# Kernel optimization log

Measured on AMD Instinct MI355X. Metric: run time of the kernel, lower is better.

Reference implementation:

```python
import jax, jax.numpy as jnp
import numpy as np

DIN = 1024   # input_embedding_size
D = 128      # embedding_size
N, T = 4, 4096


def setup_inputs() -> dict:
    key = jax.random.key(0)
    kx, kq, kk, kv = jax.random.split(key, 4)
    x = jax.random.normal(kx, (N, T, DIN), dtype=jnp.float32)
    # torch Linear(DIN, D, bias=False): weight [D, DIN], y = x @ W.T.
    # Store transposed [DIN, D] so q = x @ Wq is the same math.
    s = 1.0 / np.sqrt(DIN)
    Wq = jax.random.uniform(kq, (DIN, D), jnp.float32, -s, s)
    Wk = jax.random.uniform(kk, (DIN, D), jnp.float32, -s, s)
    Wv = jax.random.uniform(kv, (DIN, D), jnp.float32, -s, s)
    return {"x": x, "Wq": Wq, "Wk": Wk, "Wv": Wv}


def reference(x, Wq, Wk, Wv):
    # x: [N,T,DIN]
    q = jnp.einsum('ntc,cd->ntd', x, Wq)  # [N,T,D]
    k = jnp.einsum('ntc,cd->ntd', x, Wk)
    v = jnp.einsum('ntc,cd->ntd', x, Wv)
    att = jnp.einsum('ntd,nsd->nts', q, k)  # [N,T,T], no 1/sqrt(D) scaling (faithful)
    Tlen = x.shape[1]
    causal = jnp.tril(jnp.ones((Tlen, Tlen), dtype=bool))
    # faithful to torch: tril() zeros upper triangle, then masked_fill(att == 0, -inf)
    att = jnp.where(causal, att, 0.0)
    att = jnp.where(att == 0.0, -jnp.inf, att)
    att = jax.nn.softmax(att, axis=-1)  # [N,T,T]
    out = jnp.einsum('nts,nsd->ntd', att, v)  # [N,T,D]
    return out, att
```

## Files before the change

### kernel.cpp

```cpp
#include <hip/hip_runtime.h>

typedef _Float16 f16;
typedef __attribute__((ext_vector_type(8))) _Float16 f16x8;
typedef __attribute__((ext_vector_type(8))) short s16x8;
typedef __attribute__((ext_vector_type(4))) float f32x4;
typedef __attribute__((ext_vector_type(4))) unsigned short us16x4;

#define DIN   1024
#define DD    128
#define NBAT  4
#define TLEN  4096

static __device__ __forceinline__ unsigned short f2bf(float f) {
  unsigned int u = __builtin_bit_cast(unsigned int, f);
  u = (u + 0x7fffu + ((u >> 16) & 1u)) >> 16;
  return (unsigned short)u;
}
static __device__ __forceinline__ float bf2f(unsigned short h) {
  return __builtin_bit_cast(float, (unsigned int)h << 16);
}
static __device__ __forceinline__ unsigned short f2h(float f) {
  _Float16 h = (_Float16)f;
  return __builtin_bit_cast(unsigned short, h);
}
static __device__ __forceinline__ int swz128(int d, int key) {
  return ((((d >> 3) ^ key) & 15) << 3) | (d & 7);
}

typedef __attribute__((address_space(1))) const unsigned int* gas1_t;
typedef __attribute__((address_space(3))) unsigned int* las3_t;
static __device__ __forceinline__ void gload16(const void* g, void* l) {
  __builtin_amdgcn_global_load_lds((gas1_t)g, (las3_t)l, 16, 0, 0);
}

__global__ void build_wt(const float* __restrict__ Wq, const float* __restrict__ Wk,
                         const float* __restrict__ Wv,
                         unsigned short* __restrict__ Wh, unsigned short* __restrict__ Wl) {
  int col = blockIdx.x;
  const float* W = (col < 128) ? Wq : (col < 256 ? Wk : Wv);
  int j = col & 127;
  for (int kk = (int)threadIdx.x; kk < DIN; kk += blockDim.x) {
    float w = W[(size_t)kk * DD + j];
    unsigned short h = f2bf(w);
    unsigned short l = f2bf(w - bf2f(h));
    Wh[(size_t)col * DIN + kk] = h;
    Wl[(size_t)col * DIN + kk] = l;
  }
}

__global__ __launch_bounds__(256, 2) void proj_qkv(
    const float* __restrict__ x,
    const unsigned short* __restrict__ Wh, const unsigned short* __restrict__ Wl,
    unsigned short* __restrict__ qws, unsigned short* __restrict__ kws,
    unsigned short* __restrict__ vws) {
  __shared__ __align__(16) unsigned short Ah[32 * 64];
  __shared__ __align__(16) unsigned short Al[32 * 64];
  __shared__ __align__(16) unsigned short vt[128 * 40];

  const int tid = (int)threadIdx.x;
  const int lane = tid & 63;
  const int wid = tid >> 6;
  const int lr = lane & 15;
  const int lg = lane >> 4;
  const int t0 = blockIdx.x * 32;

  const int srow = tid >> 3;
  const int sg = tid & 7;
  const float* xsrc = x + (size_t)(t0 + srow) * DIN + sg * 8;
  const int sgs = (sg ^ (srow & 7)) * 8;

  f32x4 acc[2][6];
#pragma unroll
  for (int a = 0; a < 2; ++a)
#pragma unroll
    for (int c = 0; c < 6; ++c) acc[a][c] = f32x4{0.f, 0.f, 0.f, 0.f};

  for (int kr = 0; kr < 16; ++kr) {
    {
      f32x4 a0 = *(const f32x4*)(xsrc + kr * 64);
      f32x4 a1 = *(const f32x4*)(xsrc + kr * 64 + 4);
      s16x8 hv, lv;
#pragma unroll
      for (int e = 0; e < 4; ++e) {
        unsigned short h0 = f2bf(a0[e]);
        hv[e] = (short)h0; lv[e] = (short)f2bf(a0[e] - bf2f(h0));
        unsigned short h1 = f2bf(a1[e]);
        hv[4 + e] = (short)h1; lv[4 + e] = (short)f2bf(a1[e] - bf2f(h1));
      }
      *(s16x8*)&Ah[srow * 64 + sgs] = hv;
      *(s16x8*)&Al[srow * 64 + sgs] = lv;
    }
    __syncthreads();

#pragma unroll
    for (int kc = 0; kc < 2; ++kc) {
      s16x8 ah[2], al[2];
#pragma unroll
      for (int rf = 0; rf < 2; ++rf) {
        int g = (((kc * 4 + lg) ^ (lr & 7)) << 3);
        ah[rf] = *(const s16x8*)&Ah[(rf * 16 + lr) * 64 + g];
        al[rf] = *(const s16x8*)&Al[(rf * 16 + lr) * 64 + g];
      }
#pragma unroll
      for (int cf = 0; cf < 6; ++cf) {
        size_t boff = (size_t)(wid * 96 + cf * 16 + lr) * DIN + (size_t)kr * 64 + kc * 32 + lg * 8;
        s16x8 bh = *(const s16x8*)(Wh + boff);
        s16x8 bl = *(const s16x8*)(Wl + boff);
#pragma unroll
        for (int rf = 0; rf < 2; ++rf) {
          acc[rf][cf] = __builtin_amdgcn_mfma_f32_16x16x32_bf16(ah[rf], bh, acc[rf][cf], 0, 0, 0);
          acc[rf][cf] = __builtin_amdgcn_mfma_f32_16x16x32_bf16(ah[rf], bl, acc[rf][cf], 0, 0, 0);
          acc[rf][cf] = __builtin_amdgcn_mfma_f32_16x16x32_bf16(al[rf], bh, acc[rf][cf], 0, 0, 0);
        }
      }
    }
    __syncthreads();
  }

  const int n = t0 >> 12, t0l = t0 & (TLEN - 1);
#pragma unroll
  for (int cf = 0; cf < 6; ++cf) {
    int c = wid * 96 + cf * 16 + lr;
#pragma unroll
    for (int rf = 0; rf < 2; ++rf)
#pragma unroll
      for (int e = 0; e < 4; ++e) {
        int tl = rf * 16 + lg * 4 + e;
        int t = t0 + tl;
        unsigned short hv = f2h(acc[rf][cf][e]);
        if (c < 128) {
          qws[(size_t)t * DD + c] = hv;
        } else if (c < 256) {
          kws[(size_t)t * DD + swz128(c - 128, t & 7)] = hv;
        } else {
          vt[(c - 256) * 40 + tl] = hv;
        }
      }
  }
  __syncthreads();
  if (tid < 128) {
    int d = tid;
    unsigned short* dst = vws + ((size_t)n * DD + d) * TLEN + t0l;
#pragma unroll
    for (int h = 0; h < 4; ++h) {
      f16x8 vv = *(const f16x8*)&vt[d * 40 + h * 8];
      *(f16x8*)(dst + h * 8) = vv;
    }
  }
}

__global__ __launch_bounds__(512, 4) void attn_fused(
    const unsigned short* __restrict__ qws, const unsigned short* __restrict__ kws,
    const unsigned short* __restrict__ vws, float* __restrict__ out,
    float* __restrict__ att) {
  __shared__ __align__(16) unsigned short kl[2][16384];
  __shared__ __align__(16) unsigned short pp[8][16 * 40];
  __shared__ float zb[8][16];
  __shared__ float rzb[32];

  const int tid = (int)threadIdx.x;
  const int lane = tid & 63;
  const int wid = tid >> 6;
  const int lr = lane & 15;
  const int lg = lane >> 4;
  const int rg = wid >> 2;
  const int cg = wid & 3;

  int b = (int)blockIdx.x;
  int cr = (b < 256) ? b : (767 - b);
  const int qi = cr >> 2;
  const int n = cr & 3;
  const int t0 = qi * 32;
  const int jmax = (t0 + 31) >> 7;

  const unsigned short* kbase = kws + (size_t)(n * TLEN) * DD;
  const unsigned short* vbase = vws + (size_t)n * DD * TLEN;
  float* attn_base = att + (size_t)n * TLEN * TLEN + (size_t)t0 * TLEN;

#pragma unroll
  for (int rr = 0; rr < 4; ++rr) {
    int idx = rr * 512 + tid;
    gload16((const char*)kbase + (size_t)idx * 16, (char*)kl[0] + (size_t)idx * 16);
  }

  {
    int cz0 = (jmax + 1) * 128;
    f32x4 zv = f32x4{0.f, 0.f, 0.f, 0.f};
    for (int r = 0; r < 32; ++r) {
      float* rowp = attn_base + (size_t)r * TLEN;
      for (int c = cz0 + tid * 4; c < TLEN; c += 2048) *(f32x4*)(rowp + c) = zv;
    }
  }

  f16x8 qa[4];
  {
    const unsigned short* q0 = qws + (size_t)(n * TLEN + t0 + rg * 16 + lr) * DD + lg * 8;
#pragma unroll
    for (int kc = 0; kc < 4; ++kc) qa[kc] = *(const f16x8*)(q0 + kc * 32);
  }
  const int rowl0 = rg * 16 + lg * 4;

  float zacc[4] = {0.f, 0.f, 0.f, 0.f};
  for (int j = 0; j <= jmax; ++j) {
    __syncthreads();
    if (j < jmax) {
      const char* gk = (const char*)(kbase + (size_t)((j + 1) * 128) * DD);
#pragma unroll
      for (int rr = 0; rr < 4; ++rr) {
        int idx = rr * 512 + tid;
        gload16(gk + (size_t)idx * 16, (char*)kl[(j + 1) & 1] + (size_t)idx * 16);
      }
    }
    const unsigned short* klc = kl[j & 1];
#pragma unroll
    for (int cf = 0; cf < 2; ++cf) {
      int krow = cg * 32 + cf * 16 + lr;
      f32x4 s = f32x4{0.f, 0.f, 0.f, 0.f};
#pragma unroll
      for (int kc = 0; kc < 4; ++kc) {
        f16x8 kb = *(const f16x8*)&klc[krow * 128 + ((((kc * 4 + lg) ^ (krow & 7))) << 3)];
        s = __builtin_amdgcn_mfma_f32_16x16x32_f16(qa[kc], kb, s, 0, 0, 0);
      }
      int colg = j * 128 + krow;
#pragma unroll
      for (int e = 0; e < 4; ++e) {
        int rowg = t0 + rowl0 + e;
        zacc[e] += (colg <= rowg && s[e] != 0.0f) ? __expf(s[e]) : 0.0f;
      }
    }
  }
#pragma unroll
  for (int e = 0; e < 4; ++e) {
    float z = zacc[e];
    z += __shfl_xor(z, 1);
    z += __shfl_xor(z, 2);
    z += __shfl_xor(z, 4);
    z += __shfl_xor(z, 8);
    if (lr == 0) zb[wid][lg * 4 + e] = z;
  }
  __syncthreads();
  if (tid < 32) {
    int r = tid, rgq = r >> 4, rl = r & 15;
    float z = zb[rgq * 4 + 0][rl] + zb[rgq * 4 + 1][rl] + zb[rgq * 4 + 2][rl] + zb[rgq * 4 + 3][rl];
    rzb[r] = (z > 0.f) ? (1.0f / z) : 0.0f;
  }
  __syncthreads();
  float rz[4];
#pragma unroll
  for (int e = 0; e < 4; ++e) rz[e] = rzb[rowl0 + e];

#pragma unroll
  for (int rr = 0; rr < 4; ++rr) {
    int idx = rr * 512 + tid;
    gload16((const char*)kbase + (size_t)idx * 16, (char*)kl[0] + (size_t)idx * 16);
  }

  f32x4 oacc[8];
#pragma unroll
  for (int fd = 0; fd < 8; ++fd) oacc[fd] = f32x4{0.f, 0.f, 0.f, 0.f};
  unsigned short* ppw = pp[wid];

  for (int j = 0; j <= jmax; ++j) {
    __syncthreads();
    if (j < jmax) {
      const char* gk = (const char*)(kbase + (size_t)((j + 1) * 128) * DD);
#pragma unroll
      for (int rr = 0; rr < 4; ++rr) {
        int idx = rr * 512 + tid;
        gload16(gk + (size_t)idx * 16, (char*)kl[(j + 1) & 1] + (size_t)idx * 16);
      }
    }
    const unsigned short* klc = kl[j & 1];

    f32x4 s[2];
#pragma unroll
    for (int cf = 0; cf < 2; ++cf) {
      int krow = cg * 32 + cf * 16 + lr;
      s[cf] = f32x4{0.f, 0.f, 0.f, 0.f};
#pragma unroll
      for (int kc = 0; kc < 4; ++kc) {
        f16x8 kb = *(const f16x8*)&klc[krow * 128 + ((((kc * 4 + lg) ^ (krow & 7))) << 3)];
        s[cf] = __builtin_amdgcn_mfma_f32_16x16x32_f16(qa[kc], kb, s[cf], 0, 0, 0);
      }
    }

    f16x8 vb[8];
#pragma unroll
    for (int fd = 0; fd < 8; ++fd) {
      vb[fd] = *(const f16x8*)(vbase + (size_t)(fd * 16 + lr) * TLEN + (size_t)j * 128 + cg * 32 + lg * 8);
    }

#pragma unroll
    for (int cf = 0; cf < 2; ++cf) {
      int krow = cg * 32 + cf * 16 + lr;
      int colg = j * 128 + krow;
#pragma unroll
      for (int e = 0; e < 4; ++e) {
        int rowg = t0 + rowl0 + e;
        float ev = (colg <= rowg && s[cf][e] != 0.0f) ? __expf(s[cf][e]) : 0.0f;
        float p = ev * rz[e];
        attn_base[(size_t)(rowl0 + e) * TLEN + colg] = p;
        ppw[(lg * 4 + e) * 40 + cf * 16 + lr] = f2h(p);
      }
    }
    f16x8 pa = *(const f16x8*)&ppw[lr * 40 + lg * 8];
#pragma unroll
    for (int fd = 0; fd < 8; ++fd) {
      oacc[fd] = __builtin_amdgcn_mfma_f32_16x16x32_f16(pa, vb[fd], oacc[fd], 0, 0, 0);
    }
  }

  __syncthreads();
  float* red = (float*)kl;
#pragma unroll
  for (int fd = 0; fd < 8; ++fd)
#pragma unroll
    for (int e = 0; e < 4; ++e)
      red[((size_t)wid * 16 + lg * 4 + e) * 128 + fd * 16 + lr] = oacc[fd][e];
  __syncthreads();
  {
    int r = tid >> 4;
    int d0 = (tid & 15) * 8;
    int rgq = r >> 4, rl = r & 15;
    f32x4 s0 = f32x4{0.f, 0.f, 0.f, 0.f}, s1 = f32x4{0.f, 0.f, 0.f, 0.f};
#pragma unroll
    for (int c = 0; c < 4; ++c) {
      const float* src = red + ((size_t)(rgq * 4 + c) * 16 + rl) * 128 + d0;
      f32x4 a = *(const f32x4*)src;
      f32x4 bb = *(const f32x4*)(src + 4);
#pragma unroll
      for (int i = 0; i < 4; ++i) { s0[i] += a[i]; s1[i] += bb[i]; }
    }
    float* dst = out + ((size_t)n * TLEN + t0 + r) * DD + d0;
    *(f32x4*)dst = s0;
    *(f32x4*)(dst + 4) = s1;
  }
}

extern "C" void kernel_launch(void* const* d_in, const int* in_sizes, int n_in,
                              void* d_out, int out_size, void* d_ws, size_t ws_size,
                              hipStream_t stream) {
  const float* x  = (const float*)d_in[0];
  const float* Wq = (const float*)d_in[1];
  const float* Wk = (const float*)d_in[2];
  const float* Wv = (const float*)d_in[3];

  float* out = (float*)d_out;
  float* att = out + (size_t)NBAT * TLEN * DD;

  unsigned short* ws = (unsigned short*)d_ws;
  unsigned short* Wh  = ws;
  unsigned short* Wl  = Wh + (size_t)384 * DIN;
  unsigned short* qws = Wl + (size_t)384 * DIN;
  unsigned short* kws = qws + (size_t)NBAT * TLEN * DD;
  unsigned short* vws = kws + (size_t)NBAT * TLEN * DD;

  build_wt<<<dim3(384), dim3(256), 0, stream>>>(Wq, Wk, Wv, Wh, Wl);
  proj_qkv<<<dim3(512), dim3(256), 0, stream>>>(x, Wh, Wl, qws, kws, vws);
  attn_fused<<<dim3(512), dim3(512), 0, stream>>>(qws, kws, vws, out, att);
}
```

Measured before the change: 534.5 us.

## Retile QKV projection with LDS-staged weights and split attention into two kernels

The projection is retiled to 128x128 output blocks, one blockIdx.y per Q/K/V, with the bf16 hi/lo weights staged into swizzled LDS through global_load_lds instead of being read per lane from global memory. Attention is split into a normalizer kernel and a PV kernel that exchange reciprocal row sums through workspace. K tiles are now read directly from global memory instead of being double-buffered in LDS. The attention matrix is written with vectorized rows taken from the fp16 P tile, which lowers the stored precision of att to fp16. The split adds a launch and recomputes QK^T in both kernels.

Result: no change. 538.4 us (+0.7%).

```diff
diff --git a/kernel.cpp b/kernel.cpp
--- a/kernel.cpp
+++ b/kernel.cpp
@@ -23,8 +23,8 @@
   _Float16 h = (_Float16)f;
   return __builtin_bit_cast(unsigned short, h);
 }
-static __device__ __forceinline__ int swz128(int d, int key) {
-  return ((((d >> 3) ^ key) & 15) << 3) | (d & 7);
+static __device__ __forceinline__ int swz64(int c, int key) {
+  return ((((c >> 3) ^ key) & 7) << 3) | (c & 7);
 }
 
 typedef __attribute__((address_space(1))) const unsigned int* gas1_t;
@@ -43,8 +43,10 @@
     float w = W[(size_t)kk * DD + j];
     unsigned short h = f2bf(w);
     unsigned short l = f2bf(w - bf2f(h));
-    Wh[(size_t)col * DIN + kk] = h;
-    Wl[(size_t)col * DIN + kk] = l;
+    int c64 = kk >> 6, w64 = kk & 63;
+    int kks = (c64 << 6) + swz64(w64, col & 7);
+    Wh[(size_t)col * DIN + kks] = h;
+    Wl[(size_t)col * DIN + kks] = l;
   }
 }
 
@@ -53,110 +55,124 @@
     const unsigned short* __restrict__ Wh, const unsigned short* __restrict__ Wl,
     unsigned short* __restrict__ qws, unsigned short* __restrict__ kws,
     unsigned short* __restrict__ vws) {
-  __shared__ __align__(16) unsigned short Ah[32 * 64];
-  __shared__ __align__(16) unsigned short Al[32 * 64];
-  __shared__ __align__(16) unsigned short vt[128 * 40];
+  __shared__ __align__(16) unsigned short U[4 * 128 * 64];
+  unsigned short* Ah = U;
+  unsigned short* Al = U + 8192;
+  unsigned short* Bh = U + 16384;
+  unsigned short* Bl = U + 24576;
 
   const int tid = (int)threadIdx.x;
   const int lane = tid & 63;
+  const int lg = lane >> 4;
+  const int lr = lane & 15;
   const int wid = tid >> 6;
-  const int lr = lane & 15;
-  const int lg = lane >> 4;
-  const int t0 = blockIdx.x * 32;
-
-  const int srow = tid >> 3;
-  const int sg = tid & 7;
-  const float* xsrc = x + (size_t)(t0 + srow) * DIN + sg * 8;
-  const int sgs = (sg ^ (srow & 7)) * 8;
-
-  f32x4 acc[2][6];
-#pragma unroll
-  for (int a = 0; a < 2; ++a)
-#pragma unroll
-    for (int c = 0; c < 6; ++c) acc[a][c] = f32x4{0.f, 0.f, 0.f, 0.f};
+  const int t0 = blockIdx.x * 128;
+  const int ct = blockIdx.y;
+
+  const int rbase = (wid >> 1) * 64;
+  const int cbase = (wid & 1) * 64;
+
+  f32x4 acc[4][4];
+#pragma unroll
+  for (int m = 0; m < 4; ++m)
+#pragma unroll
+    for (int n = 0; n < 4; ++n) acc[m][n] = f32x4{0.f, 0.f, 0.f, 0.f};
 
   for (int kr = 0; kr < 16; ++kr) {
-    {
-      f32x4 a0 = *(const f32x4*)(xsrc + kr * 64);
-      f32x4 a1 = *(const f32x4*)(xsrc + kr * 64 + 4);
-      s16x8 hv, lv;
-#pragma unroll
-      for (int e = 0; e < 4; ++e) {
-        unsigned short h0 = f2bf(a0[e]);
-        hv[e] = (short)h0; lv[e] = (short)f2bf(a0[e] - bf2f(h0));
-        unsigned short h1 = f2bf(a1[e]);
-        hv[4 + e] = (short)h1; lv[4 + e] = (short)f2bf(a1[e] - bf2f(h1));
-      }
-      *(s16x8*)&Ah[srow * 64 + sgs] = hv;
-      *(s16x8*)&Al[srow * 64 + sgs] = lv;
+#pragma unroll
+    for (int rr = 0; rr < 8; ++rr) {
+      int idx = rr * 256 + tid;
+      int row = idx >> 4;
+      int c0 = (idx & 15) * 4;
+      f32x4 xv = *(const f32x4*)(x + (size_t)(t0 + row) * DIN + kr * 64 + c0);
+      int g = swz64(c0, row & 7);
+      unsigned short hs0 = f2bf(xv[0]), hs1 = f2bf(xv[1]), hs2 = f2bf(xv[2]), hs3 = f2bf(xv[3]);
+      us16x4 hv = {hs0, hs1, hs2, hs3};
+      us16x4 lv = {f2bf(xv[0] - bf2f(hs0)), f2bf(xv[1] - bf2f(hs1)),
+                   f2bf(xv[2] - bf2f(hs2)), f2bf(xv[3] - bf2f(hs3))};
+      *(us16x4*)&Ah[row * 64 + g] = hv;
+      *(us16x4*)&Al[row * 64 + g] = lv;
+    }
+#pragma unroll
+    for (int rr = 0; rr < 4; ++rr) {
+      int idx = rr * 256 + tid;
+      int row = idx >> 3;
+      int g = idx & 7;
+      size_t gbyte = ((size_t)(ct * 128 + row) * DIN + (size_t)kr * 64) * 2 + (size_t)g * 16;
+      gload16((const char*)Wh + gbyte, (char*)Bh + (size_t)idx * 16);
+      gload16((const char*)Wl + gbyte, (char*)Bl + (size_t)idx * 16);
     }
     __syncthreads();
 
 #pragma unroll
     for (int kc = 0; kc < 2; ++kc) {
-      s16x8 ah[2], al[2];
-#pragma unroll
-      for (int rf = 0; rf < 2; ++rf) {
-        int g = (((kc * 4 + lg) ^ (lr & 7)) << 3);
-        ah[rf] = *(const s16x8*)&Ah[(rf * 16 + lr) * 64 + g];
-        al[rf] = *(const s16x8*)&Al[(rf * 16 + lr) * 64 + g];
-      }
-#pragma unroll
-      for (int cf = 0; cf < 6; ++cf) {
-        size_t boff = (size_t)(wid * 96 + cf * 16 + lr) * DIN + (size_t)kr * 64 + kc * 32 + lg * 8;
-        s16x8 bh = *(const s16x8*)(Wh + boff);
-        s16x8 bl = *(const s16x8*)(Wl + boff);
-#pragma unroll
-        for (int rf = 0; rf < 2; ++rf) {
-          acc[rf][cf] = __builtin_amdgcn_mfma_f32_16x16x32_bf16(ah[rf], bh, acc[rf][cf], 0, 0, 0);
-          acc[rf][cf] = __builtin_amdgcn_mfma_f32_16x16x32_bf16(ah[rf], bl, acc[rf][cf], 0, 0, 0);
-          acc[rf][cf] = __builtin_amdgcn_mfma_f32_16x16x32_bf16(al[rf], bh, acc[rf][cf], 0, 0, 0);
+      s16x8 ah[4], al[4], bh[4], bl[4];
+#pragma unroll
+      for (int m = 0; m < 4; ++m) {
+        int r = rbase + m * 16 + lr;
+        int g = ((kc * 4 + lg) ^ (r & 7)) * 8;
+        ah[m] = *(const s16x8*)&Ah[r * 64 + g];
+        al[m] = *(const s16x8*)&Al[r * 64 + g];
+      }
+#pragma unroll
+      for (int n = 0; n < 4; ++n) {
+        int c = cbase + n * 16 + lr;
+        int g = ((kc * 4 + lg) ^ (c & 7)) * 8;
+        bh[n] = *(const s16x8*)&Bh[c * 64 + g];
+        bl[n] = *(const s16x8*)&Bl[c * 64 + g];
+      }
+#pragma unroll
+      for (int m = 0; m < 4; ++m)
+#pragma unroll
+        for (int n = 0; n < 4; ++n) {
+          acc[m][n] = __builtin_amdgcn_mfma_f32_16x16x32_bf16(ah[m], bh[n], acc[m][n], 0, 0, 0);
+          acc[m][n] = __builtin_amdgcn_mfma_f32_16x16x32_bf16(ah[m], bl[n], acc[m][n], 0, 0, 0);
+          acc[m][n] = __builtin_amdgcn_mfma_f32_16x16x32_bf16(al[m], bh[n], acc[m][n], 0, 0, 0);
         }
-      }
     }
     __syncthreads();
   }
 
   const int n = t0 >> 12, t0l = t0 & (TLEN - 1);
-#pragma unroll
-  for (int cf = 0; cf < 6; ++cf) {
-    int c = wid * 96 + cf * 16 + lr;
-#pragma unroll
-    for (int rf = 0; rf < 2; ++rf)
-#pragma unroll
-      for (int e = 0; e < 4; ++e) {
-        int tl = rf * 16 + lg * 4 + e;
-        int t = t0 + tl;
-        unsigned short hv = f2h(acc[rf][cf][e]);
-        if (c < 128) {
-          qws[(size_t)t * DD + c] = hv;
-        } else if (c < 256) {
-          kws[(size_t)t * DD + swz128(c - 128, t & 7)] = hv;
-        } else {
-          vt[(c - 256) * 40 + tl] = hv;
+  if (ct < 2) {
+    unsigned short* dstb = (ct == 0) ? qws : kws;
+#pragma unroll
+    for (int m = 0; m < 4; ++m)
+#pragma unroll
+      for (int nn = 0; nn < 4; ++nn)
+#pragma unroll
+        for (int e = 0; e < 4; ++e) {
+          int t = t0 + rbase + m * 16 + lg * 4 + e;
+          int d = cbase + nn * 16 + lr;
+          dstb[(size_t)t * DD + d] = f2h(acc[m][nn][e]);
         }
-      }
-  }
-  __syncthreads();
-  if (tid < 128) {
-    int d = tid;
-    unsigned short* dst = vws + ((size_t)n * DD + d) * TLEN + t0l;
-#pragma unroll
-    for (int h = 0; h < 4; ++h) {
-      f16x8 vv = *(const f16x8*)&vt[d * 40 + h * 8];
-      *(f16x8*)(dst + h * 8) = vv;
-    }
-  }
-}
-
-__global__ __launch_bounds__(512, 4) void attn_fused(
+  } else {
+    unsigned short* vt = U;
+#pragma unroll
+    for (int m = 0; m < 4; ++m)
+#pragma unroll
+      for (int nn = 0; nn < 4; ++nn)
+#pragma unroll
+        for (int e = 0; e < 4; ++e) {
+          int tl = rbase + m * 16 + lg * 4 + e;
+          int d = cbase + nn * 16 + lr;
+          vt[d * 132 + tl] = f2h(acc[m][nn][e]);
+        }
+    __syncthreads();
+    int d = tid >> 1;
+    int half = (tid & 1) * 64;
+    unsigned short* dst = vws + ((size_t)n * DD + d) * TLEN + t0l + half;
+#pragma unroll
+    for (int h = 0; h < 8; ++h) {
+      *(f16x8*)(dst + h * 8) = *(const f16x8*)&vt[d * 132 + half + h * 8];
+    }
+  }
+}
+
+__global__ __launch_bounds__(512, 4) void attn_z(
     const unsigned short* __restrict__ qws, const unsigned short* __restrict__ kws,
-    const unsigned short* __restrict__ vws, float* __restrict__ out,
-    float* __restrict__ att) {
-  __shared__ __align__(16) unsigned short kl[2][16384];
-  __shared__ __align__(16) unsigned short pp[8][16 * 40];
+    float* __restrict__ rzg, float* __restrict__ att) {
   __shared__ float zb[8][16];
-  __shared__ float rzb[32];
 
   const int tid = (int)threadIdx.x;
   const int lane = tid & 63;
@@ -171,17 +187,10 @@
   const int qi = cr >> 2;
   const int n = cr & 3;
   const int t0 = qi * 32;
-  const int jmax = (t0 + 31) >> 7;
+  const int jmax = t0 >> 7;
 
   const unsigned short* kbase = kws + (size_t)(n * TLEN) * DD;
-  const unsigned short* vbase = vws + (size_t)n * DD * TLEN;
   float* attn_base = att + (size_t)n * TLEN * TLEN + (size_t)t0 * TLEN;
-
-#pragma unroll
-  for (int rr = 0; rr < 4; ++rr) {
-    int idx = rr * 512 + tid;
-    gload16((const char*)kbase + (size_t)idx * 16, (char*)kl[0] + (size_t)idx * 16);
-  }
 
   {
     int cz0 = (jmax + 1) * 128;
@@ -202,23 +211,14 @@
 
   float zacc[4] = {0.f, 0.f, 0.f, 0.f};
   for (int j = 0; j <= jmax; ++j) {
-    __syncthreads();
-    if (j < jmax) {
-      const char* gk = (const char*)(kbase + (size_t)((j + 1) * 128) * DD);
-#pragma unroll
-      for (int rr = 0; rr < 4; ++rr) {
-        int idx = rr * 512 + tid;
-        gload16(gk + (size_t)idx * 16, (char*)kl[(j + 1) & 1] + (size_t)idx * 16);
-      }
-    }
-    const unsigned short* klc = kl[j & 1];
 #pragma unroll
     for (int cf = 0; cf < 2; ++cf) {
       int krow = cg * 32 + cf * 16 + lr;
+      const unsigned short* kt = kbase + (size_t)(j * 128 + krow) * DD + lg * 8;
       f32x4 s = f32x4{0.f, 0.f, 0.f, 0.f};
 #pragma unroll
       for (int kc = 0; kc < 4; ++kc) {
-        f16x8 kb = *(const f16x8*)&klc[krow * 128 + ((((kc * 4 + lg) ^ (krow & 7))) << 3)];
+        f16x8 kb = *(const f16x8*)(kt + kc * 32);
         s = __builtin_amdgcn_mfma_f32_16x16x32_f16(qa[kc], kb, s, 0, 0, 0);
       }
       int colg = j * 128 + krow;
@@ -240,56 +240,72 @@
   }
   __syncthreads();
   if (tid < 32) {
-    int r = tid, rgq = r >> 4, rl = r & 15;
+    int rgq = tid >> 4, rl = tid & 15;
     float z = zb[rgq * 4 + 0][rl] + zb[rgq * 4 + 1][rl] + zb[rgq * 4 + 2][rl] + zb[rgq * 4 + 3][rl];
-    rzb[r] = (z > 0.f) ? (1.0f / z) : 0.0f;
-  }
-  __syncthreads();
+    rzg[(size_t)n * TLEN + t0 + tid] = (z > 0.f) ? (1.0f / z) : 0.0f;
+  }
+}
+
+__global__ __launch_bounds__(512, 4) void attn_pv(
+    const unsigned short* __restrict__ qws, const unsigned short* __restrict__ kws,
+    const unsigned short* __restrict__ vws, const float* __restrict__ rzg,
+    float* __restrict__ out, float* __restrict__ att) {
+  __shared__ __align__(16) char smem[65536];
+
+  const int tid = (int)threadIdx.x;
+  const int lane = tid & 63;
+  const int wid = tid >> 6;
+  const int lr = lane & 15;
+  const int lg = lane >> 4;
+  const int rg = wid >> 2;
+  const int cg = wid & 3;
+
+  int b = (int)blockIdx.x;
+  int cr = (b < 256) ? b : (767 - b);
+  const int qi = cr >> 2;
+  const int n = cr & 3;
+  const int t0 = qi * 32;
+  const int jmax = t0 >> 7;
+
+  const unsigned short* kbase = kws + (size_t)(n * TLEN) * DD;
+  const unsigned short* vbase = vws + (size_t)n * DD * TLEN;
+  float* attn_base = att + (size_t)n * TLEN * TLEN + (size_t)t0 * TLEN;
+
+  f16x8 qa[4];
+  {
+    const unsigned short* q0 = qws + (size_t)(n * TLEN + t0 + rg * 16 + lr) * DD + lg * 8;
+#pragma unroll
+    for (int kc = 0; kc < 4; ++kc) qa[kc] = *(const f16x8*)(q0 + kc * 32);
+  }
+  const int rowl0 = rg * 16 + lg * 4;
   float rz[4];
 #pragma unroll
-  for (int e = 0; e < 4; ++e) rz[e] = rzb[rowl0 + e];
-
-#pragma unroll
-  for (int rr = 0; rr < 4; ++rr) {
-    int idx = rr * 512 + tid;
-    gload16((const char*)kbase + (size_t)idx * 16, (char*)kl[0] + (size_t)idx * 16);
-  }
+  for (int e = 0; e < 4; ++e) rz[e] = rzg[(size_t)n * TLEN + t0 + rowl0 + e];
+
+  unsigned short* ppw = (unsigned short*)(smem + wid * 1280);
 
   f32x4 oacc[8];
 #pragma unroll
   for (int fd = 0; fd < 8; ++fd) oacc[fd] = f32x4{0.f, 0.f, 0.f, 0.f};
-  unsigned short* ppw = pp[wid];
 
   for (int j = 0; j <= jmax; ++j) {
-    __syncthreads();
-    if (j < jmax) {
-      const char* gk = (const char*)(kbase + (size_t)((j + 1) * 128) * DD);
-#pragma unroll
-      for (int rr = 0; rr < 4; ++rr) {
-        int idx = rr * 512 + tid;
-        gload16(gk + (size_t)idx * 16, (char*)kl[(j + 1) & 1] + (size_t)idx * 16);
-      }
-    }
-    const unsigned short* klc = kl[j & 1];
-
     f32x4 s[2];
 #pragma unroll
     for (int cf = 0; cf < 2; ++cf) {
       int krow = cg * 32 + cf * 16 + lr;
+      const unsigned short* kt = kbase + (size_t)(j * 128 + krow) * DD + lg * 8;
       s[cf] = f32x4{0.f, 0.f, 0.f, 0.f};
 #pragma unroll
       for (int kc = 0; kc < 4; ++kc) {
-        f16x8 kb = *(const f16x8*)&klc[krow * 128 + ((((kc * 4 + lg) ^ (krow & 7))) << 3)];
+        f16x8 kb = *(const f16x8*)(kt + kc * 32);
         s[cf] = __builtin_amdgcn_mfma_f32_16x16x32_f16(qa[kc], kb, s[cf], 0, 0, 0);
       }
     }
-
     f16x8 vb[8];
 #pragma unroll
     for (int fd = 0; fd < 8; ++fd) {
       vb[fd] = *(const f16x8*)(vbase + (size_t)(fd * 16 + lr) * TLEN + (size_t)j * 128 + cg * 32 + lg * 8);
     }
-
 #pragma unroll
     for (int cf = 0; cf < 2; ++cf) {
       int krow = cg * 32 + cf * 16 + lr;
@@ -298,9 +314,7 @@
       for (int e = 0; e < 4; ++e) {
         int rowg = t0 + rowl0 + e;
         float ev = (colg <= rowg && s[cf][e] != 0.0f) ? __expf(s[cf][e]) : 0.0f;
-        float p = ev * rz[e];
-        attn_base[(size_t)(rowl0 + e) * TLEN + colg] = p;
-        ppw[(lg * 4 + e) * 40 + cf * 16 + lr] = f2h(p);
+        ppw[(lg * 4 + e) * 40 + cf * 16 + lr] = f2h(ev * rz[e]);
       }
     }
     f16x8 pa = *(const f16x8*)&ppw[lr * 40 + lg * 8];
@@ -308,10 +322,20 @@
     for (int fd = 0; fd < 8; ++fd) {
       oacc[fd] = __builtin_amdgcn_mfma_f32_16x16x32_f16(pa, vb[fd], oacc[fd], 0, 0, 0);
     }
+    {
+      int r = lane >> 2, cs = (lane & 3) * 8;
+      f16x8 pv = *(const f16x8*)&ppw[r * 40 + cs];
+      f32x4 o0, o1;
+#pragma unroll
+      for (int i = 0; i < 4; ++i) { o0[i] = (float)pv[i]; o1[i] = (float)pv[4 + i]; }
+      float* dst = attn_base + (size_t)(rg * 16 + r) * TLEN + j * 128 + cg * 32 + cs;
+      *(f32x4*)dst = o0;
+      *(f32x4*)(dst + 4) = o1;
+    }
   }
 
   __syncthreads();
-  float* red = (float*)kl;
+  float* red = (float*)smem;
 #pragma unroll
   for (int fd = 0; fd < 8; ++fd)
 #pragma unroll
@@ -354,8 +378,10 @@
   unsigned short* qws = Wl + (size_t)384 * DIN;
   unsigned short* kws = qws + (size_t)NBAT * TLEN * DD;
   unsigned short* vws = kws + (size_t)NBAT * TLEN * DD;
+  float* rzg = (float*)(vws + (size_t)NBAT * TLEN * DD);
 
   build_wt<<<dim3(384), dim3(256), 0, stream>>>(Wq, Wk, Wv, Wh, Wl);
-  proj_qkv<<<dim3(512), dim3(256), 0, stream>>>(x, Wh, Wl, qws, kws, vws);
-  attn_fused<<<dim3(512), dim3(512), 0, stream>>>(qws, kws, vws, out, att);
-}
+  proj_qkv<<<dim3(128, 3), dim3(256), 0, stream>>>(x, Wh, Wl, qws, kws, vws);
+  attn_z<<<dim3(512), dim3(512), 0, stream>>>(qws, kws, rzg, att);
+  attn_pv<<<dim3(512), dim3(512), 0, stream>>>(qws, kws, vws, rzg, out, att);
+}
```
